# Kernel optimization log

Measured on AMD Instinct MI355X. Metric: run time of the kernel, lower is better.

## Reference

```python
import jax, jax.numpy as jnp
import numpy as np

NEG = -1e6  # masked_softmax fill value from the torch source


def setup_inputs() -> dict:
    key = jax.random.key(0)
    ks = jax.random.split(key, 7)
    B, NQ, NK, D, H = 4, 256, 1024, 256, 256
    queries = jax.random.normal(ks[0], (B, NQ, D), dtype=jnp.float32)
    keys_ = jax.random.normal(ks[1], (B, NK, D), dtype=jnp.float32)
    values = jax.random.normal(ks[2], (B, NK, D), dtype=jnp.float32)
    valid_lens = jax.random.randint(ks[3], (B,), 1, NK + 1, dtype=jnp.int32)
    scale = 1.0 / np.sqrt(D)
    Wq = jax.random.normal(ks[4], (D, H), dtype=jnp.float32) * scale
    Wk = jax.random.normal(ks[5], (D, H), dtype=jnp.float32) * scale
    w_v = jax.random.normal(ks[6], (H,), dtype=jnp.float32) * (1.0 / np.sqrt(H))
    return {"queries": queries, "keys": keys_, "values": values,
            "valid_lens": valid_lens, "Wq": Wq, "Wk": Wk, "w_v": w_v}


def reference(queries, keys, values, valid_lens, Wq, Wk, w_v):
    # projections
    q = jnp.einsum('bqd,dh->bqh', queries, Wq)           # [B,NQ,H]
    k = jnp.einsum('bkd,dh->bkh', keys, Wk)              # [B,NK,H]
    # broadcast-add + tanh + dense(->1): scores [B,NQ,NK]
    features = jnp.tanh(q[:, :, None, :] + k[:, None, :, :])  # [B,NQ,NK,H]
    scores = jnp.einsum('bqkh,h->bqk', features, w_v)
    # masked softmax over last axis with per-batch valid lengths
    nk = keys.shape[1]
    mask = jnp.arange(nk)[None, None, :] < valid_lens[:, None, None]  # [B,1,NK]
    scores = jnp.where(mask, scores, NEG)
    attn = jax.nn.softmax(scores, axis=-1)               # [B,NQ,NK]
    # dropout in eval mode -> identity
    return jnp.einsum('bqk,bkd->bqd', attn, values)      # [B,NQ,D]
```

## Files before the change

kernel.cpp:

```cpp
#include <hip/hip_runtime.h>
#include <hip/hip_fp16.h>
#include <math.h>

#define BB 4
#define NQ 256
#define NK 1024
#define DD 256
#define HH 256

typedef __attribute__((ext_vector_type(8))) _Float16 f16x8;
typedef __attribute__((ext_vector_type(4))) _Float16 f16x4;
typedef __attribute__((ext_vector_type(4))) float f32x4;

__global__ __launch_bounds__(256) void proj_mfma_kernel(
    const float* __restrict__ Q, const float* __restrict__ K,
    const float* __restrict__ Wq, const float* __restrict__ Wk,
    const int* __restrict__ vlen,
    __half* __restrict__ Eq, __half* __restrict__ Ek)
{
    int bx = blockIdx.x;
    int mt = bx >> 3, nt = bx & 7;
    const float *A, *W; __half* C; int bm;
    if (mt < 16) { A = Q; W = Wq; C = Eq; bm = mt * 64; }
    else {
        int kt = mt - 16;
        int b = kt >> 4;
        int lr = (kt & 15) * 64;
        if (lr >= vlen[b]) return;
        A = K; W = Wk; C = Ek; bm = kt * 64;
    }
    int bn = nt * 32;

    __shared__ __half Wt[32][260];

    int tid = threadIdx.x;
    {
        int dp = tid >> 3, cg = tid & 7;
#pragma unroll
        for (int pp = 0; pp < 4; ++pp) {
            int d0r = (dp + pp * 32) * 2;
            float4 r0 = *(const float4*)&W[(size_t)d0r * HH + bn + cg * 4];
            float4 r1 = *(const float4*)&W[(size_t)(d0r + 1) * HH + bn + cg * 4];
            int n = cg * 4;
            *(__half2*)&Wt[n + 0][d0r] = __floats2half2_rn(r0.x, r1.x);
            *(__half2*)&Wt[n + 1][d0r] = __floats2half2_rn(r0.y, r1.y);
            *(__half2*)&Wt[n + 2][d0r] = __floats2half2_rn(r0.z, r1.z);
            *(__half2*)&Wt[n + 3][d0r] = __floats2half2_rn(r0.w, r1.w);
        }
    }
    __syncthreads();

    int lane = tid & 63, w = tid >> 6;
    int wm = w & 1, wn = w >> 1;
    int lm = lane & 15, lk = (lane >> 4) * 4;

    const float* arow0 = A + (size_t)(bm + wm * 32 + lm) * DD;
    const float* arow1 = arow0 + (size_t)16 * DD;
    const __half* brow = &Wt[wn * 16 + lm][0];

    f32x4 acc0 = {0.f, 0.f, 0.f, 0.f};
    f32x4 acc1 = {0.f, 0.f, 0.f, 0.f};

    float4 a00 = *(const float4*)(arow0 + lk);
    float4 a01 = *(const float4*)(arow0 + 16 + lk);
    float4 a10 = *(const float4*)(arow1 + lk);
    float4 a11 = *(const float4*)(arow1 + 16 + lk);
    f16x4 b0 = *(const f16x4*)&brow[lk];
    f16x4 b1 = *(const f16x4*)&brow[16 + lk];

#pragma unroll
    for (int s = 0; s < 8; ++s) {
        float4 c00 = a00, c01 = a01, c10 = a10, c11 = a11;
        f16x4 cb0 = b0, cb1 = b1;
        if (s < 7) {
            int d = (s + 1) * 32;
            a00 = *(const float4*)(arow0 + d + lk);
            a01 = *(const float4*)(arow0 + d + 16 + lk);
            a10 = *(const float4*)(arow1 + d + lk);
            a11 = *(const float4*)(arow1 + d + 16 + lk);
            b0 = *(const f16x4*)&brow[d + lk];
            b1 = *(const f16x4*)&brow[d + 16 + lk];
        }
        f16x8 af0, af1, bf;
        af0[0] = (_Float16)c00.x; af0[1] = (_Float16)c00.y;
        af0[2] = (_Float16)c00.z; af0[3] = (_Float16)c00.w;
        af0[4] = (_Float16)c01.x; af0[5] = (_Float16)c01.y;
        af0[6] = (_Float16)c01.z; af0[7] = (_Float16)c01.w;
        af1[0] = (_Float16)c10.x; af1[1] = (_Float16)c10.y;
        af1[2] = (_Float16)c10.z; af1[3] = (_Float16)c10.w;
        af1[4] = (_Float16)c11.x; af1[5] = (_Float16)c11.y;
        af1[6] = (_Float16)c11.z; af1[7] = (_Float16)c11.w;
        bf[0] = cb0[0]; bf[1] = cb0[1]; bf[2] = cb0[2]; bf[3] = cb0[3];
        bf[4] = cb1[0]; bf[5] = cb1[1]; bf[6] = cb1[2]; bf[7] = cb1[3];
        acc0 = __builtin_amdgcn_mfma_f32_16x16x32_f16(af0, bf, acc0, 0, 0, 0);
        acc1 = __builtin_amdgcn_mfma_f32_16x16x32_f16(af1, bf, acc1, 0, 0, 0);
    }

    int mB0 = bm + wm * 32 + (lane >> 4) * 4;
    int mB1 = mB0 + 16;
    int n = bn + wn * 16 + lm;
#pragma unroll
    for (int r = 0; r < 4; ++r) {
        float e0 = __expf(2.f * fminf(fmaxf(acc0[r], -5.5f), 5.5f));
        float e1 = __expf(2.f * fminf(fmaxf(acc1[r], -5.5f), 5.5f));
        C[(size_t)(mB0 + r) * HH + n] = __float2half(e0);
        C[(size_t)(mB1 + r) * HH + n] = __float2half(e1);
    }
}

__global__ __launch_bounds__(256) void scores_kernel(
    const __half* __restrict__ Eq, const __half* __restrict__ Ek,
    const float* __restrict__ wv, const int* __restrict__ vlen,
    float* __restrict__ P, float* __restrict__ Psum)
{
    __shared__ __align__(16) __half sQ[32][HH + 8];
    __shared__ __align__(16) __half sK[32][HH + 8];
    __shared__ __align__(16) float sW[HH];

    int bid = blockIdx.x;
    int b = bid & 3;
    int rest = bid >> 2;
    int qc = rest & 7;
    int kc = rest >> 3;
    int L = vlen[b];
    int k0 = kc * 32;
    if (k0 >= L) return;
    int q0 = qc * 32;

    int tid = threadIdx.x;
    {
        int c8 = tid & 31;
        int r0 = tid >> 5;
        const __half* gq = Eq + ((size_t)b * NQ + q0) * HH;
        const __half* gk = Ek + ((size_t)b * NK + k0) * HH;
#pragma unroll
        for (int i = 0; i < 4; ++i) {
            int r = r0 + 8 * i;
            *(uint4*)&sQ[r][c8 * 8] = *(const uint4*)&gq[(size_t)r * HH + c8 * 8];
            *(uint4*)&sK[r][c8 * 8] = *(const uint4*)&gk[(size_t)r * HH + c8 * 8];
        }
        sW[tid] = wv[tid];
    }
    __syncthreads();

    int ki = tid & 15, qi = tid >> 4;
    float a00 = 0.f, a01 = 0.f, a10 = 0.f, a11 = 0.f;

#pragma unroll 4
    for (int h4 = 0; h4 < HH / 4; ++h4) {
        float4 w = *(const float4*)&sW[h4 * 4];
        float2 q0a = __half22float2(*(const __half2*)&sQ[qi][h4 * 4]);
        float2 q0b = __half22float2(*(const __half2*)&sQ[qi][h4 * 4 + 2]);
        float2 q1a = __half22float2(*(const __half2*)&sQ[qi + 16][h4 * 4]);
        float2 q1b = __half22float2(*(const __half2*)&sQ[qi + 16][h4 * 4 + 2]);
        float2 k0a = __half22float2(*(const __half2*)&sK[ki][h4 * 4]);
        float2 k0b = __half22float2(*(const __half2*)&sK[ki][h4 * 4 + 2]);
        float2 k1a = __half22float2(*(const __half2*)&sK[ki + 16][h4 * 4]);
        float2 k1b = __half22float2(*(const __half2*)&sK[ki + 16][h4 * 4 + 2]);
        float4 A0 = {q0a.x, q0a.y, q0b.x, q0b.y};
        float4 A1 = {q1a.x, q1a.y, q1b.x, q1b.y};
        float4 B0 = {k0a.x, k0a.y, k0b.x, k0b.y};
        float4 B1 = {k1a.x, k1a.y, k1b.x, k1b.y};
#define PAIR4(acc, Aq, Bk)                                                   \
        {                                                                    \
            float d1 = fmaf(Aq.x, Bk.x, 1.f);                                \
            float d2 = fmaf(Aq.y, Bk.y, 1.f);                                \
            float n12 = fmaf(w.y, d1, w.x * d2);                             \
            acc = fmaf(n12, __builtin_amdgcn_rcpf(d1 * d2), acc);            \
            float d3 = fmaf(Aq.z, Bk.z, 1.f);                                \
            float d4 = fmaf(Aq.w, Bk.w, 1.f);                                \
            float n34 = fmaf(w.w, d3, w.z * d4);                             \
            acc = fmaf(n34, __builtin_amdgcn_rcpf(d3 * d4), acc);            \
        }
        PAIR4(a00, A0, B0);
        PAIR4(a01, A0, B1);
        PAIR4(a10, A1, B0);
        PAIR4(a11, A1, B1);
#undef PAIR4
    }

    int kA = k0 + ki, kB = kA + 16;
    float p00 = (kA < L) ? __expf(-2.f * a00) : 0.f;
    float p10 = (kA < L) ? __expf(-2.f * a10) : 0.f;
    float p01 = (kB < L) ? __expf(-2.f * a01) : 0.f;
    float p11 = (kB < L) ? __expf(-2.f * a11) : 0.f;

    float* s0 = P + ((size_t)b * NQ + q0 + qi) * NK;
    float* s1 = P + ((size_t)b * NQ + q0 + qi + 16) * NK;
    s0[kA] = p00; s0[kB] = p01;
    s1[kA] = p10; s1[kB] = p11;

    float r0s = p00 + p01, r1s = p10 + p11;
#pragma unroll
    for (int o = 1; o <= 8; o <<= 1) {
        r0s += __shfl_xor(r0s, o, 64);
        r1s += __shfl_xor(r1s, o, 64);
    }
    if (ki == 0) {
        Psum[((size_t)b * NQ + q0 + qi) * 32 + kc] = r0s;
        Psum[((size_t)b * NQ + q0 + qi + 16) * 32 + kc] = r1s;
    }
}

__global__ __launch_bounds__(256) void pv_kernel(
    const float* __restrict__ P, const float* __restrict__ V,
    const float* __restrict__ Psum, const int* __restrict__ vlen,
    float* __restrict__ out)
{
    __shared__ __align__(16) float sPt[2][32][18];
    __shared__ __align__(16) float sV[2][32][36];
    __shared__ float sAll[3][64][9];
    __shared__ float sRowsum[16];

    int bid = blockIdx.x;
    int b = bid & 3;
    int rest = bid >> 2;
    int qt = rest >> 3, dt = rest & 7;
    int q0 = qt * 16, d0 = dt * 32;
    int L = vlen[b];
    int nc = (L + 31) >> 5;

    int tid = threadIdx.x;
    if (tid < 16) {
        float s = 0.f;
        const float* pp = Psum + ((size_t)b * NQ + q0 + tid) * 32;
        for (int c = 0; c < nc; ++c) s += pp[c];
        sRowsum[tid] = s;
    }

    bool isP = tid < 128;
    int pr = tid >> 3, pc4 = tid & 7;
    int vt = tid & 127;
    int vr = vt >> 2, vc = (vt & 3) * 2;

    int w = tid >> 6, sp = tid & 63;
    int qg = sp >> 3, dg = sp & 7;

    const float* Pb = P + ((size_t)b * NQ + q0 + pr) * NK;
    const float* Vb = V + (size_t)b * NK * DD + d0;

    float4 pf = {0,0,0,0}, vfa = {0,0,0,0}, vfb = {0,0,0,0};
    if (isP) pf = *(const float4*)(Pb + pc4 * 4);
    else {
        vfa = *(const float4*)(Vb + (size_t)vr * DD + vc * 4);
        vfb = *(const float4*)(Vb + (size_t)vr * DD + vc * 4 + 4);
    }

    float acc[2][4] = {};

    for (int c = 0; c < nc; ++c) {
        int cur = c & 1;
        if (isP) {
            sPt[cur][pc4 * 4 + 0][pr] = pf.x;
            sPt[cur][pc4 * 4 + 1][pr] = pf.y;
            sPt[cur][pc4 * 4 + 2][pr] = pf.z;
            sPt[cur][pc4 * 4 + 3][pr] = pf.w;
        } else {
            *(float4*)&sV[cur][vr][vc * 4] = vfa;
            *(float4*)&sV[cur][vr][vc * 4 + 4] = vfb;
        }
        if (c + 1 < nc) {
            int kn = (c + 1) * 32;
            if (isP) pf = *(const float4*)(Pb + kn + pc4 * 4);
            else {
                vfa = *(const float4*)(Vb + (size_t)(kn + vr) * DD + vc * 4);
                vfb = *(const float4*)(Vb + (size_t)(kn + vr) * DD + vc * 4 + 4);
            }
        }
        __syncthreads();
#pragma unroll
        for (int kk = 0; kk < 8; ++kk) {
            float2 A  = *(const float2*)&sPt[cur][w * 8 + kk][qg * 2];
            float4 Bv = *(const float4*)&sV[cur][w * 8 + kk][dg * 4];
            acc[0][0] = fmaf(A.x, Bv.x, acc[0][0]);
            acc[0][1] = fmaf(A.x, Bv.y, acc[0][1]);
            acc[0][2] = fmaf(A.x, Bv.z, acc[0][2]);
            acc[0][3] = fmaf(A.x, Bv.w, acc[0][3]);
            acc[1][0] = fmaf(A.y, Bv.x, acc[1][0]);
            acc[1][1] = fmaf(A.y, Bv.y, acc[1][1]);
            acc[1][2] = fmaf(A.y, Bv.z, acc[1][2]);
            acc[1][3] = fmaf(A.y, Bv.w, acc[1][3]);
        }
    }

    if (w > 0) {
#pragma unroll
        for (int i = 0; i < 2; ++i)
#pragma unroll
            for (int j = 0; j < 4; ++j) sAll[w - 1][sp][i * 4 + j] = acc[i][j];
    }
    __syncthreads();
    if (w == 0) {
#pragma unroll
        for (int ww = 0; ww < 3; ++ww)
#pragma unroll
            for (int i = 0; i < 2; ++i)
#pragma unroll
                for (int j = 0; j < 4; ++j) acc[i][j] += sAll[ww][sp][i * 4 + j];
#pragma unroll
        for (int i = 0; i < 2; ++i) {
            float inv = 1.0f / sRowsum[qg * 2 + i];
            float4 o = { acc[i][0] * inv, acc[i][1] * inv,
                         acc[i][2] * inv, acc[i][3] * inv };
            *(float4*)&out[((size_t)b * NQ + q0 + qg * 2 + i) * DD + d0 + dg * 4] = o;
        }
    }
}

extern "C" void kernel_launch(void* const* d_in, const int* in_sizes, int n_in,
                              void* d_out, int out_size, void* d_ws, size_t ws_size,
                              hipStream_t stream) {
    const float* queries = (const float*)d_in[0];
    const float* keys    = (const float*)d_in[1];
    const float* values  = (const float*)d_in[2];
    const int*   vlens   = (const int*)d_in[3];
    const float* Wq      = (const float*)d_in[4];
    const float* Wk      = (const float*)d_in[5];
    const float* wv      = (const float*)d_in[6];
    float* out = (float*)d_out;

    __half* Eqh = (__half*)d_ws;
    __half* Ekh = Eqh + (size_t)BB * NQ * HH;
    float*  P    = (float*)(Ekh + (size_t)BB * NK * HH);
    float*  Psum = P + (size_t)BB * NQ * NK;

    proj_mfma_kernel<<<dim3(640), 256, 0, stream>>>(
        queries, keys, Wq, Wk, vlens, Eqh, Ekh);

    scores_kernel<<<dim3(BB * (NQ / 32) * (NK / 32)), 256, 0, stream>>>(
        Eqh, Ekh, wv, vlens, P, Psum);

    pv_kernel<<<dim3(BB * (NQ / 16) * (DD / 32)), 256, 0, stream>>>(
        P, values, Psum, vlens, out);
}
```

Measured before the change: 52.85 us.

## Fuse PV product into scores kernel with split-K partial outputs and combine pass

Each scores block now multiplies its 32x32 probability tile, held in shared memory, by the matching 32-row slice of V and writes a partial 32x256 output, instead of storing P to global memory. A new combine kernel sums the partials over key chunks and normalises by the row sum. This drops the global round trip of P and the separate PV kernel's tiling. In exchange it writes and reads a large partial-output buffer (up to 32 chunks x full D per query row) and V is read directly from global memory with no shared-memory staging.

```diff
diff --git a/kernel.cpp b/kernel.cpp
--- a/kernel.cpp
+++ b/kernel.cpp
@@ -108,14 +108,16 @@
     }
 }
 
-__global__ __launch_bounds__(256) void scores_kernel(
+__global__ __launch_bounds__(256) void scorespv_kernel(
     const __half* __restrict__ Eq, const __half* __restrict__ Ek,
     const float* __restrict__ wv, const int* __restrict__ vlen,
-    float* __restrict__ P, float* __restrict__ Psum)
+    const float* __restrict__ V,
+    float* __restrict__ Opart, float* __restrict__ Psum)
 {
     __shared__ __align__(16) __half sQ[32][HH + 8];
     __shared__ __align__(16) __half sK[32][HH + 8];
     __shared__ __align__(16) float sW[HH];
+    __shared__ __align__(16) float sP[32][34];
 
     int bid = blockIdx.x;
     int b = bid & 3;
@@ -185,10 +187,10 @@
     float p01 = (kB < L) ? __expf(-2.f * a01) : 0.f;
     float p11 = (kB < L) ? __expf(-2.f * a11) : 0.f;
 
-    float* s0 = P + ((size_t)b * NQ + q0 + qi) * NK;
-    float* s1 = P + ((size_t)b * NQ + q0 + qi + 16) * NK;
-    s0[kA] = p00; s0[kB] = p01;
-    s1[kA] = p10; s1[kB] = p11;
+    sP[ki][qi]           = p00;
+    sP[ki + 16][qi]      = p01;
+    sP[ki][qi + 16]      = p10;
+    sP[ki + 16][qi + 16] = p11;
 
     float r0s = p00 + p01, r1s = p10 + p11;
 #pragma unroll
@@ -200,111 +202,70 @@
         Psum[((size_t)b * NQ + q0 + qi) * 32 + kc] = r0s;
         Psum[((size_t)b * NQ + q0 + qi + 16) * 32 + kc] = r1s;
     }
-}
-
-__global__ __launch_bounds__(256) void pv_kernel(
-    const float* __restrict__ P, const float* __restrict__ V,
-    const float* __restrict__ Psum, const int* __restrict__ vlen,
-    float* __restrict__ out)
+
+    __syncthreads();
+
+    int qp = tid >> 4;
+    int dp = tid & 15;
+    const float4* Vb4 = (const float4*)(V + ((size_t)b * NK + k0) * DD);
+
+    float4 acc0[4] = {{0,0,0,0},{0,0,0,0},{0,0,0,0},{0,0,0,0}};
+    float4 acc1[4] = {{0,0,0,0},{0,0,0,0},{0,0,0,0},{0,0,0,0}};
+
+#pragma unroll 2
+    for (int k = 0; k < 32; ++k) {
+        float2 p = *(const float2*)&sP[k][qp * 2];
+#pragma unroll
+        for (int j = 0; j < 4; ++j) {
+            float4 v = Vb4[(size_t)k * 64 + j * 16 + dp];
+            acc0[j].x = fmaf(p.x, v.x, acc0[j].x);
+            acc0[j].y = fmaf(p.x, v.y, acc0[j].y);
+            acc0[j].z = fmaf(p.x, v.z, acc0[j].z);
+            acc0[j].w = fmaf(p.x, v.w, acc0[j].w);
+            acc1[j].x = fmaf(p.y, v.x, acc1[j].x);
+            acc1[j].y = fmaf(p.y, v.y, acc1[j].y);
+            acc1[j].z = fmaf(p.y, v.z, acc1[j].z);
+            acc1[j].w = fmaf(p.y, v.w, acc1[j].w);
+        }
+    }
+
+    size_t base = (((size_t)(b * 8 + qc) * 32 + kc) * 32 + qp * 2) * (size_t)DD;
+    float4* op0 = (float4*)(Opart + base);
+    float4* op1 = (float4*)(Opart + base + DD);
+#pragma unroll
+    for (int j = 0; j < 4; ++j) {
+        op0[j * 16 + dp] = acc0[j];
+        op1[j * 16 + dp] = acc1[j];
+    }
+}
+
+__global__ __launch_bounds__(256) void combine_kernel(
+    const float* __restrict__ Opart, const float* __restrict__ Psum,
+    const int* __restrict__ vlen, float* __restrict__ out)
 {
-    __shared__ __align__(16) float sPt[2][32][18];
-    __shared__ __align__(16) float sV[2][32][36];
-    __shared__ float sAll[3][64][9];
-    __shared__ float sRowsum[16];
-
-    int bid = blockIdx.x;
-    int b = bid & 3;
-    int rest = bid >> 2;
-    int qt = rest >> 3, dt = rest & 7;
-    int q0 = qt * 16, d0 = dt * 32;
+    int tid = threadIdx.x;
+    int rr = tid >> 6, lane = tid & 63;
+    int row = blockIdx.x * 4 + rr;
+    int b = row >> 8;
+    int q = row & 255;
+    int qc = q >> 5, r32 = q & 31;
     int L = vlen[b];
     int nc = (L + 31) >> 5;
 
-    int tid = threadIdx.x;
-    if (tid < 16) {
-        float s = 0.f;
-        const float* pp = Psum + ((size_t)b * NQ + q0 + tid) * 32;
-        for (int c = 0; c < nc; ++c) s += pp[c];
-        sRowsum[tid] = s;
-    }
-
-    bool isP = tid < 128;
-    int pr = tid >> 3, pc4 = tid & 7;
-    int vt = tid & 127;
-    int vr = vt >> 2, vc = (vt & 3) * 2;
-
-    int w = tid >> 6, sp = tid & 63;
-    int qg = sp >> 3, dg = sp & 7;
-
-    const float* Pb = P + ((size_t)b * NQ + q0 + pr) * NK;
-    const float* Vb = V + (size_t)b * NK * DD + d0;
-
-    float4 pf = {0,0,0,0}, vfa = {0,0,0,0}, vfb = {0,0,0,0};
-    if (isP) pf = *(const float4*)(Pb + pc4 * 4);
-    else {
-        vfa = *(const float4*)(Vb + (size_t)vr * DD + vc * 4);
-        vfb = *(const float4*)(Vb + (size_t)vr * DD + vc * 4 + 4);
-    }
-
-    float acc[2][4] = {};
-
+    float s = (lane < nc) ? Psum[(size_t)row * 32 + lane] : 0.f;
+#pragma unroll
+    for (int o = 32; o; o >>= 1) s += __shfl_xor(s, o, 64);
+    float inv = 1.0f / s;
+
+    const float* opbase = Opart + ((size_t)(b * 8 + qc) * 32) * 32 * DD
+                        + (size_t)r32 * DD + lane * 4;
+    float4 o = {0.f, 0.f, 0.f, 0.f};
     for (int c = 0; c < nc; ++c) {
-        int cur = c & 1;
-        if (isP) {
-            sPt[cur][pc4 * 4 + 0][pr] = pf.x;
-            sPt[cur][pc4 * 4 + 1][pr] = pf.y;
-            sPt[cur][pc4 * 4 + 2][pr] = pf.z;
-            sPt[cur][pc4 * 4 + 3][pr] = pf.w;
-        } else {
-            *(float4*)&sV[cur][vr][vc * 4] = vfa;
-            *(float4*)&sV[cur][vr][vc * 4 + 4] = vfb;
-        }
-        if (c + 1 < nc) {
-            int kn = (c + 1) * 32;
-            if (isP) pf = *(const float4*)(Pb + kn + pc4 * 4);
-            else {
-                vfa = *(const float4*)(Vb + (size_t)(kn + vr) * DD + vc * 4);
-                vfb = *(const float4*)(Vb + (size_t)(kn + vr) * DD + vc * 4 + 4);
-            }
-        }
-        __syncthreads();
-#pragma unroll
-        for (int kk = 0; kk < 8; ++kk) {
-            float2 A  = *(const float2*)&sPt[cur][w * 8 + kk][qg * 2];
-            float4 Bv = *(const float4*)&sV[cur][w * 8 + kk][dg * 4];
-            acc[0][0] = fmaf(A.x, Bv.x, acc[0][0]);
-            acc[0][1] = fmaf(A.x, Bv.y, acc[0][1]);
-            acc[0][2] = fmaf(A.x, Bv.z, acc[0][2]);
-            acc[0][3] = fmaf(A.x, Bv.w, acc[0][3]);
-            acc[1][0] = fmaf(A.y, Bv.x, acc[1][0]);
-            acc[1][1] = fmaf(A.y, Bv.y, acc[1][1]);
-            acc[1][2] = fmaf(A.y, Bv.z, acc[1][2]);
-            acc[1][3] = fmaf(A.y, Bv.w, acc[1][3]);
-        }
-    }
-
-    if (w > 0) {
-#pragma unroll
-        for (int i = 0; i < 2; ++i)
-#pragma unroll
-            for (int j = 0; j < 4; ++j) sAll[w - 1][sp][i * 4 + j] = acc[i][j];
-    }
-    __syncthreads();
-    if (w == 0) {
-#pragma unroll
-        for (int ww = 0; ww < 3; ++ww)
-#pragma unroll
-            for (int i = 0; i < 2; ++i)
-#pragma unroll
-                for (int j = 0; j < 4; ++j) acc[i][j] += sAll[ww][sp][i * 4 + j];
-#pragma unroll
-        for (int i = 0; i < 2; ++i) {
-            float inv = 1.0f / sRowsum[qg * 2 + i];
-            float4 o = { acc[i][0] * inv, acc[i][1] * inv,
-                         acc[i][2] * inv, acc[i][3] * inv };
-            *(float4*)&out[((size_t)b * NQ + q0 + qg * 2 + i) * DD + d0 + dg * 4] = o;
-        }
-    }
+        float4 x = *(const float4*)(opbase + (size_t)c * 32 * DD);
+        o.x += x.x; o.y += x.y; o.z += x.z; o.w += x.w;
+    }
+    o.x *= inv; o.y *= inv; o.z *= inv; o.w *= inv;
+    *(float4*)&out[(size_t)row * DD + lane * 4] = o;
 }
 
 extern "C" void kernel_launch(void* const* d_in, const int* in_sizes, int n_in,
@@ -319,17 +280,17 @@
     const float* wv      = (const float*)d_in[6];
     float* out = (float*)d_out;
 
-    __half* Eqh = (__half*)d_ws;
-    __half* Ekh = Eqh + (size_t)BB * NQ * HH;
-    float*  P    = (float*)(Ekh + (size_t)BB * NK * HH);
-    float*  Psum = P + (size_t)BB * NQ * NK;
+    __half* Eqh  = (__half*)d_ws;
+    __half* Ekh  = Eqh + (size_t)BB * NQ * HH;
+    float*  Psum = (float*)(Ekh + (size_t)BB * NK * HH);
+    float*  Opart = Psum + (size_t)BB * NQ * 32;
 
     proj_mfma_kernel<<<dim3(640), 256, 0, stream>>>(
         queries, keys, Wq, Wk, vlens, Eqh, Ekh);
 
-    scores_kernel<<<dim3(BB * (NQ / 32) * (NK / 32)), 256, 0, stream>>>(
-        Eqh, Ekh, wv, vlens, P, Psum);
-
-    pv_kernel<<<dim3(BB * (NQ / 16) * (DD / 32)), 256, 0, stream>>>(
-        P, values, Psum, vlens, out);
-}
+    scorespv_kernel<<<dim3(BB * (NQ / 32) * (NK / 32)), 256, 0, stream>>>(
+        Eqh, Ekh, wv, vlens, values, Opart, Psum);
+
+    combine_kernel<<<dim3(BB * NQ / 4), 256, 0, stream>>>(
+        Opart, Psum, vlens, out);
+}
```

Measured after the change: 58.61 us. 1.11x slower.
